# Performance work log

Hardware: AMD Instinct MI355X
Metric: run time of the kernel (lower is better)

Reference implementation:

```python
import jax, jax.numpy as jnp
import numpy as np

B_, N_, D_ = 8, 1024, 64
H_, DH_ = 4, 16
DI_, DS_, DTR_ = 128, 64, 4
MAXP = 512


def _ln(x, w, b, eps=1e-5):
    m = jnp.mean(x, -1, keepdims=True)
    v = jnp.mean((x - m) ** 2, -1, keepdims=True)
    return (x - m) * jax.lax.rsqrt(v + eps) * w + b


def _attn(x, drop_mask, Wq, Wkv, Wo, bo, rel_emb):
    b, n, d = x.shape
    scale = DH_ ** -0.5
    q = (x @ Wq).reshape(b, n, H_, DH_).transpose(0, 2, 1, 3)
    kv = x @ Wkv
    k = kv[..., :d].reshape(b, n, H_, DH_).transpose(0, 2, 1, 3)
    v = kv[..., d:].reshape(b, n, H_, DH_).transpose(0, 2, 1, 3)
    dots = jnp.einsum('bhid,bhjd->bhij', q, k) * scale
    seq = jnp.arange(n)
    dist = jnp.clip(seq[:, None] - seq[None, :], -MAXP, MAXP) + MAXP
    rpe = rel_emb[dist]  # (n, n, DH_)
    dots = dots + jnp.einsum('bhid,ijd->bhij', q, rpe) * scale
    # stochastic key drop: Bernoulli(0.3) positions get -1e12
    dots = dots + drop_mask.astype(dots.dtype) * (-1e12)
    attn = jax.nn.softmax(dots, axis=-1)
    out = jnp.einsum('bhij,bhjd->bhid', attn, v)
    out = out.transpose(0, 2, 1, 3).reshape(b, n, H_ * DH_)
    return out @ Wo + bo


def _mamba(x, W_in, conv_w, conv_b, W_xproj, W_dt, b_dt, A_log, Dm, W_out):
    b, n, _ = x.shape
    xz = x @ W_in                      # (b, n, 2*DI_)
    u, z = xz[..., :DI_], xz[..., DI_:]
    uc = u.transpose(0, 2, 1)          # (b, DI_, n)
    uc = jax.lax.conv_general_dilated(
        uc, conv_w[:, None, :], (1,), ((3, 0),),
        feature_group_count=DI_, dimension_numbers=('NCH', 'OIH', 'NCH'))
    uc = uc + conv_b[None, :, None]
    u = jax.nn.silu(uc).transpose(0, 2, 1)  # (b, n, DI_)
    xdb = u @ W_xproj                  # (b, n, DTR_+2*DS_)
    dt = jax.nn.softplus(xdb[..., :DTR_] @ W_dt + b_dt)  # (b, n, DI_)
    Bm = xdb[..., DTR_:DTR_ + DS_]
    Cm = xdb[..., DTR_ + DS_:]
    A = -jnp.exp(A_log)                # (DI_, DS_)

    def step(h, inp):
        dt_t, B_t, C_t, u_t = inp      # (b,DI_),(b,DS_),(b,DS_),(b,DI_)
        dA = jnp.exp(dt_t[..., None] * A)
        h = h * dA + (dt_t * u_t)[..., None] * B_t[:, None, :]
        y = jnp.einsum('bds,bs->bd', h, C_t)
        return h, y

    h0 = jnp.zeros((b, DI_, DS_), x.dtype)
    xs = (dt.transpose(1, 0, 2), Bm.transpose(1, 0, 2),
          Cm.transpose(1, 0, 2), u.transpose(1, 0, 2))
    _, ys = jax.lax.scan(step, h0, xs)
    y = ys.transpose(1, 0, 2) + u * Dm
    y = y * jax.nn.silu(z)
    return y @ W_out


def _rmsgn(x, gamma, eps=1e-5, groups=4):
    shp = x.shape
    dpg = shp[-1] // groups
    xg = x.reshape(shp[:-1] + (groups, dpg))
    rms = jnp.sqrt(jnp.sum(xg * xg, -1, keepdims=True)) * (dpg ** -0.5)
    return (xg / (rms + eps)).reshape(shp) * gamma


def _ff1(x, c1_w, c1_b, d1_w, d1_b):
    # SwiGLUConvDeconv1d(64, 256, kernel=4, shift=1); x: (b, s2, 64)
    s2 = x.shape[1]
    xc = x.transpose(0, 2, 1)
    xc = jnp.pad(xc, ((0, 0), (0, 0), (3, 3)))
    xc = jax.lax.conv_general_dilated(
        xc, c1_w, (1,), 'VALID', dimension_numbers=('NCH', 'OIH', 'NCH'))
    xc = xc + c1_b[None, :, None]
    gate = jax.nn.silu(xc[:, 256:, :])
    xc = xc[:, :256, :] * gate
    # ConvTranspose1d stride 1 == conv with flipped kernel, full padding
    w = jnp.flip(d1_w, -1).transpose(1, 0, 2)  # (64, 256, 4)
    xc = jax.lax.conv_general_dilated(
        xc, w, (1,), ((3, 3),), dimension_numbers=('NCH', 'OIH', 'NCH'))
    xc = xc + d1_b[None, :, None]
    out = xc.transpose(0, 2, 1)
    return out[:, 3:3 + s2, :]


def _forward(x, drop_mask, ln1_w, ln1_b, Wq, Wkv, Wo, bo, rel_emb,
             ln2_w, ln2_b, W_in, conv_w, conv_b, W_xproj, W_dt, b_dt,
             A_log, Dm, W_out, gamma, c1_w, c1_b, d1_w, d1_b, ln3_w, ln3_b):
    xt = _ln(x, ln1_w, ln1_b)
    xt = _attn(xt, drop_mask, Wq, Wkv, Wo, bo, rel_emb) + x
    x = x + xt  # dropout p=0 -> identity (faithful to original residual math)
    xt = _ln(x, ln2_w, ln2_b)
    m = _mamba(xt, W_in, conv_w, conv_b, W_xproj, W_dt, b_dt, A_log, Dm, W_out)
    m = jnp.where(m >= 0, m, 0.01 * m)  # leaky_relu
    m = _rmsgn(m, gamma)
    m = m + 0.5 * _ff1(m, c1_w, c1_b, d1_w, d1_b)
    x = x + m
    return _ln(x, ln3_w, ln3_b)


def setup_inputs() -> dict:
    ks = jax.random.split(jax.random.key(0), 16)
    g = lambda i, shp, s: jax.random.normal(ks[i], shp, dtype=jnp.float32) * s
    A_log = jnp.log(jnp.tile(jnp.arange(1, DS_ + 1, dtype=jnp.float32)[None, :], (DI_, 1)))
    return {
        'x': jax.random.normal(ks[0], (B_, N_, D_), dtype=jnp.float32),
        'drop_mask': jax.random.bernoulli(ks[1], 0.3, (B_, H_, N_, N_)),
        'ln1_w': jnp.ones((D_,), jnp.float32), 'ln1_b': jnp.zeros((D_,), jnp.float32),
        'Wq': g(2, (D_, D_), 0.1), 'Wkv': g(3, (D_, 2 * D_), 0.1),
        'Wo': g(4, (D_, D_), 0.1), 'bo': jnp.zeros((D_,), jnp.float32),
        'rel_emb': g(5, (2 * MAXP + 1, DH_), 0.02),
        'ln2_w': jnp.ones((D_,), jnp.float32), 'ln2_b': jnp.zeros((D_,), jnp.float32),
        'W_in': g(6, (D_, 2 * DI_), 0.1),
        'conv_w': g(7, (DI_, 4), 0.2), 'conv_b': jnp.zeros((DI_,), jnp.float32),
        'W_xproj': g(8, (DI_, DTR_ + 2 * DS_), 0.1),
        'W_dt': g(9, (DTR_, DI_), 0.1), 'b_dt': jnp.zeros((DI_,), jnp.float32),
        'A_log': A_log, 'Dm': jnp.ones((DI_,), jnp.float32),
        'W_out': g(10, (DI_, D_), 0.1),
        'gamma': jnp.ones((D_,), jnp.float32),
        'c1_w': g(11, (512, 64, 4), 0.1), 'c1_b': jnp.zeros((512,), jnp.float32),
        'd1_w': g(12, (256, 64, 4), 0.1), 'd1_b': jnp.zeros((64,), jnp.float32),
        'ln3_w': jnp.ones((D_,), jnp.float32), 'ln3_b': jnp.zeros((D_,), jnp.float32),
    }


def reference(x, drop_mask, ln1_w, ln1_b, Wq, Wkv, Wo, bo, rel_emb,
              ln2_w, ln2_b, W_in, conv_w, conv_b, W_xproj, W_dt, b_dt,
              A_log, Dm, W_out, gamma, c1_w, c1_b, d1_w, d1_b, ln3_w, ln3_b):
    return _forward(x, drop_mask, ln1_w, ln1_b, Wq, Wkv, Wo, bo, rel_emb,
                    ln2_w, ln2_b, W_in, conv_w, conv_b, W_xproj, W_dt, b_dt,
                    A_log, Dm, W_out, gamma, c1_w, c1_b, d1_w, d1_b, ln3_w, ln3_b)
```

## Files before the change

kernel.cpp:

```cpp
#include <hip/hip_runtime.h>
#include <hip/hip_fp16.h>
#include <math.h>


__device__ __forceinline__ float wsum64(float v){
#pragma unroll
  for(int m=32;m>0;m>>=1) v += __shfl_xor(v, m, 64);
  return v;
}
__device__ __forceinline__ float wmax64(float v){
#pragma unroll
  for(int m=32;m>0;m>>=1) v = fmaxf(v, __shfl_xor(v, m, 64));
  return v;
}
__device__ __forceinline__ float silu_f(float x){ return x / (1.f + __expf(-x)); }

__global__ __launch_bounds__(256) void k_ln1_qkv(
    const float* __restrict__ x, const float* __restrict__ w1, const float* __restrict__ b1,
    const float* __restrict__ Wq, const float* __restrict__ Wkv,
    const float* __restrict__ rel, const float* __restrict__ c1w,
    const int* __restrict__ dmask,
    float* __restrict__ qb, float2* __restrict__ kvT,
    float* __restrict__ relT, float* __restrict__ c1wT,
    unsigned long long* __restrict__ mask64){
  int tid = threadIdx.x;
  int bi = blockIdx.x >> 1;
  if (blockIdx.x & 1){
    size_t base = (size_t)bi * 16384;
    const int* dp = dmask + base;
    unsigned long long* mp = mask64 + (base >> 6);
#pragma unroll 4
    for(int r=0;r<64;++r){
      int m = dp[r*256 + tid];
      unsigned long long bal = __ballot(m != 0);
      if ((tid & 63) == 0) mp[r*4 + (tid >> 6)] = bal;
    }
    return;
  }
  int lane = tid & 63, warp = tid >> 6;
  int token = bi*4 + warp;
  __shared__ float xt[4][64];
  float xv = x[(size_t)token*64 + lane];
  float mean = wsum64(xv) * 0.015625f;
  float dlt = xv - mean;
  float var = wsum64(dlt*dlt) * 0.015625f;
  float xn = dlt * rsqrtf(var + 1e-5f) * w1[lane] + b1[lane];
  xt[warp][lane] = xn;
  __syncthreads();
  float aq=0.f, ak=0.f, av=0.f;
#pragma unroll 4
  for(int dd=0; dd<64; ++dd){
    float xd = xt[warp][dd];
    aq += xd * Wq[dd*64 + lane];
    ak += xd * Wkv[dd*128 + lane];
    av += xd * Wkv[dd*128 + 64 + lane];
  }
  int b = token >> 10, i = token & 1023;
  int h = lane >> 4, dh = lane & 15;
  size_t o  = (((size_t)(b*4 + h))*1024 + i)*16 + dh;
  size_t oT = (((size_t)(b*4 + h))*16 + dh)*1024 + i;
  qb[o]=aq;
  kvT[oT] = make_float2(ak, av);

  if (bi < 65){
    int idx = bi*256 + tid;
    if (idx < 16*1025){
      int c = idx / 1025;
      int d = idx - c*1025;
      relT[idx] = rel[d*16 + c];
    }
  } else if (bi < 577){
    int idx = (bi-65)*256 + tid;
    int row = idx >> 9;
    int ii  = idx & 511;
    c1wT[idx] = c1w[(size_t)ii*256 + row];
  }
}

__global__ __launch_bounds__(256) void k_kmax(
    const float2* __restrict__ kvT, float* __restrict__ Kmax){
  int tid = threadIdx.x;
  int bh = blockIdx.x;
  const float2* base = kvT + (size_t)bh*16*1024;
  float mx = 0.f;
#pragma unroll
  for(int r=0;r<4;++r){
    int j = tid + 256*r;
    float ss = 0.f;
#pragma unroll
    for(int c=0;c<16;++c){ float2 kv = base[c*1024 + j]; ss += kv.x*kv.x; }
    mx = fmaxf(mx, ss);
  }
  mx = wmax64(mx);
  __shared__ float red[4];
  int lane = tid&63, wv = tid>>6;
  if(lane==0) red[wv]=mx;
  __syncthreads();
  if(tid==0) Kmax[bh] = sqrtf(fmaxf(fmaxf(red[0],red[1]),fmaxf(red[2],red[3])));
}

__global__ __launch_bounds__(128, 2) void k_attn(
    const float* __restrict__ qb, const float2* __restrict__ kvT,
    const unsigned long long* __restrict__ mask64, const float* __restrict__ relT,
    const float* __restrict__ Kmax, float* __restrict__ attn_raw){
  int tid = threadIdx.x;
  int lane = tid & 63, wv = tid >> 6;
  int wg   = blockIdx.x;
  int xcd  = wg & 7;
  int slot = wg >> 3;
  int bh   = xcd*4 + (slot >> 7);
  int i0   = (slot & 127) * 8;
  int b = bh >> 2, h = bh & 3;
  int R0 = wv*4, R1 = R0+1, R2 = R0+2, R3 = R0+3;

  __shared__ __align__(16) __half Gc[8][1040];
  __shared__ float qs[8][16];
  __shared__ float G0s[8], G1024s[8];
  __shared__ float gmS[8];
  __shared__ float Ms[8];
  __shared__ float sums[8];

  {
    int r = tid >> 4, c = tid & 15;
    qs[r][c] = qb[((size_t)bh*1024 + i0 + r)*16 + c] * 0.25f;
  }
  __syncthreads();

#pragma unroll 1
  for(int bb=0; bb<9; ++bb){
    int d = tid + 128*bb;
    if (d <= 1024){
      float rl[16];
#pragma unroll
      for(int c=0;c<16;++c) rl[c] = relT[c*1025 + d];
#pragma unroll
      for(int r=0;r<8;++r){
        float g = 0.f;
#pragma unroll
        for(int c=0;c<16;++c) g += qs[r][c]*rl[c];
        if (d == 0)        G0s[r] = g;
        else if (d == 1024) G1024s[r] = g;
        else {
          int j = i0 + r + 512 - d;
          if (j >= 0 && j < 1024) Gc[r][j] = __float2half_rn(g);
        }
      }
    }
  }
  __syncthreads();
  {
    const unsigned long long* mrow = mask64 + ((size_t)bh*1024 + i0)*16;
#pragma unroll 1
    for(int r=0;r<8;++r){
      float g0 = G0s[r], g1 = G1024s[r];
      int lo = i0 + r - 512;
      int hi = i0 + r + 512;
#pragma unroll
      for(int p=0;p<8;++p){
        int j = tid + 128*p;
        unsigned long long w = mrow[r*16 + (j>>6)];
        float g;
        if (j >= hi) g = g0;
        else if (j <= lo) g = g1;
        else g = __half2float(Gc[r][j]);
        if ((w >> (j & 63)) & 1ULL) g = -60000.f;
        Gc[r][j] = __float2half_rn(g);
      }
    }
  }
  __syncthreads();
  {
    int r = tid >> 4, l4 = tid & 15;
    float gm = -3.0e38f;
#pragma unroll
    for(int k=0;k<64;++k) gm = fmaxf(gm, __half2float(Gc[r][l4 + 16*k]));
#pragma unroll
    for(int m=1;m<16;m<<=1) gm = fmaxf(gm, __shfl_xor(gm, m, 64));
    if (l4 == 0) gmS[r] = gm;
  }
  __syncthreads();
  if (tid < 8){
    float qn = 0.f;
#pragma unroll
    for(int c=0;c<16;++c) qn += qs[tid][c]*qs[tid][c];
    Ms[tid] = gmS[tid] + sqrtf(qn)*Kmax[bh];
  }
  __syncthreads();

  float q0[16], q1[16], q2[16], q3[16];
#pragma unroll
  for(int c=0;c<16;++c){ q0[c]=qs[R0][c]; q1[c]=qs[R1][c]; q2[c]=qs[R2][c]; q3[c]=qs[R3][c]; }
  float M0 = Ms[R0], M1 = Ms[R1], M2 = Ms[R2], M3 = Ms[R3];

  const float2* kvb = kvT + (size_t)bh*16*1024;

  float s0=0.f, s1=0.f, s2=0.f, s3=0.f;
  float a0[16], a1[16], a2[16], a3[16];
#pragma unroll
  for(int c=0;c<16;++c){ a0[c]=0.f; a1[c]=0.f; a2[c]=0.f; a3[c]=0.f; }

  float2 kvA[16], kvB[16];
  int j = lane;
#pragma unroll
  for(int c=0;c<16;++c) kvA[c] = kvb[c*1024 + j];

#define ATTN_STEP(KV, JJ) do {                                              \
    float sv0 = __half2float(Gc[R0][JJ]), sv1 = __half2float(Gc[R1][JJ]);   \
    float sv2 = __half2float(Gc[R2][JJ]), sv3 = __half2float(Gc[R3][JJ]);   \
    _Pragma("unroll")                                                       \
    for(int c=0;c<16;++c){                                                  \
      float kx = KV[c].x;                                                   \
      sv0 += q0[c]*kx; sv1 += q1[c]*kx; sv2 += q2[c]*kx; sv3 += q3[c]*kx;   \
    }                                                                       \
    float p0 = __expf(sv0 - M0), p1 = __expf(sv1 - M1);                     \
    float p2 = __expf(sv2 - M2), p3 = __expf(sv3 - M3);                     \
    s0 += p0; s1 += p1; s2 += p2; s3 += p3;                                 \
    _Pragma("unroll")                                                       \
    for(int c=0;c<16;++c){                                                  \
      float vy = KV[c].y;                                                   \
      a0[c] += p0*vy; a1[c] += p1*vy; a2[c] += p2*vy; a3[c] += p3*vy;       \
    }                                                                       \
  } while(0)

#pragma unroll 1
  for(int t=0;t<16;t+=2){
    int jb = (j + 64) & 1023;
#pragma unroll
    for(int c=0;c<16;++c) kvB[c] = kvb[c*1024 + jb];
    ATTN_STEP(kvA, j);
    int ja = (jb + 64) & 1023;
#pragma unroll
    for(int c=0;c<16;++c) kvA[c] = kvb[c*1024 + ja];
    ATTN_STEP(kvB, jb);
    j = ja;
  }
#undef ATTN_STEP

  s0 = wsum64(s0); s1 = wsum64(s1); s2 = wsum64(s2); s3 = wsum64(s3);
#pragma unroll
  for(int c=0;c<16;++c){
    float x0 = a0[c]; x0 += __shfl_xor(x0,32,64); x0 += __shfl_xor(x0,16,64); a0[c] = x0;
    float x1 = a1[c]; x1 += __shfl_xor(x1,32,64); x1 += __shfl_xor(x1,16,64); a1[c] = x1;
    float x2 = a2[c]; x2 += __shfl_xor(x2,32,64); x2 += __shfl_xor(x2,16,64); a2[c] = x2;
    float x3 = a3[c]; x3 += __shfl_xor(x3,32,64); x3 += __shfl_xor(x3,16,64); a3[c] = x3;
  }
  __syncthreads();
  float* red = (float*)&Gc[0][0];
  if (lane < 16){
#pragma unroll
    for(int c=0;c<16;++c){
      red[R0*272 + lane*17 + c] = a0[c];
      red[R1*272 + lane*17 + c] = a1[c];
      red[R2*272 + lane*17 + c] = a2[c];
      red[R3*272 + lane*17 + c] = a3[c];
    }
  }
  if (lane == 0){ sums[R0]=s0; sums[R1]=s1; sums[R2]=s2; sums[R3]=s3; }
  __syncthreads();
  {
    int row = tid >> 4, c = tid & 15;
    float tot = 0.f;
#pragma unroll
    for(int g=0; g<16; ++g) tot += red[row*272 + g*17 + c];
    attn_raw[((size_t)b*1024 + i0 + row)*64 + h*16 + c] = tot / sums[row];
  }
}

__global__ __launch_bounds__(256) void k_post_attn(
    const float* __restrict__ x, const float* __restrict__ attn_raw,
    const float* __restrict__ Wo, const float* __restrict__ bo,
    const float* __restrict__ ln2w, const float* __restrict__ ln2b,
    const float* __restrict__ W_in,
    float* __restrict__ x2, float* __restrict__ u0, float* __restrict__ zsarr){
  int tid = threadIdx.x;
  int lane = tid & 63, wv = tid >> 6;
  int tok0 = blockIdx.x * 16;
  __shared__ float arS[16][64];
  __shared__ float lnS[16][64];
  for(int l = tid; l < 1024; l += 256)
    arS[l >> 6][l & 63] = attn_raw[(size_t)tok0*64 + l];
  __syncthreads();
#pragma unroll 1
  for(int tt = 0; tt < 4; ++tt){
    int tl = wv*4 + tt;
    int token = tok0 + tl;
    float acc = bo[lane];
#pragma unroll 4
    for(int dd = 0; dd < 64; ++dd) acc += arS[tl][dd] * Wo[dd*64 + lane];
    float t = 2.f*x[(size_t)token*64 + lane] + acc;
    x2[(size_t)token*64 + lane] = t;
    float mean = wsum64(t)*0.015625f;
    float dlt = t - mean;
    float var = wsum64(dlt*dlt)*0.015625f;
    lnS[tl][lane] = dlt*rsqrtf(var+1e-5f)*ln2w[lane] + ln2b[lane];
  }
  __syncthreads();
  int oc = tid;
  float w[64];
#pragma unroll
  for(int dd = 0; dd < 64; ++dd) w[dd] = W_in[dd*256 + oc];
  const float4* lnS4 = (const float4*)&lnS[0][0];
#pragma unroll 1
  for(int tl = 0; tl < 16; ++tl){
    float acc = 0.f;
#pragma unroll
    for(int d4 = 0; d4 < 16; ++d4){
      float4 l4 = lnS4[tl*16 + d4];
      acc += l4.x*w[4*d4] + l4.y*w[4*d4+1] + l4.z*w[4*d4+2] + l4.w*w[4*d4+3];
    }
    int token = tok0 + tl;
    if (oc < 128) u0[(size_t)token*128 + oc] = acc;
    else          zsarr[(size_t)token*128 + (oc-128)] = silu_f(acc);
  }
}

__global__ __launch_bounds__(256) void k_conv_proj(
    const float* __restrict__ u0, const float* __restrict__ conv_w, const float* __restrict__ conv_b,
    const float* __restrict__ W_xproj, const float* __restrict__ W_dt, const float* __restrict__ b_dt,
    float* __restrict__ uarr, float* __restrict__ Bmp, float* __restrict__ Cmp, float* __restrict__ dtarr){
  int sub = threadIdx.x >> 7, c = threadIdx.x & 127;
  int token = blockIdx.x*2 + sub;
  int b = token >> 10, i = token & 1023;
  __shared__ float us[2][128];
  __shared__ float dtin[2][4];
  float acc = conv_b[c];
#pragma unroll
  for(int k2=0;k2<4;++k2){
    int t2 = i - 3 + k2;
    if (t2 >= 0) acc += u0[((size_t)b*1024 + t2)*128 + c]*conv_w[c*4+k2];
  }
  float uv = silu_f(acc);
  uarr[(size_t)token*128 + c] = uv;
  us[sub][c] = uv;
  __syncthreads();
  float accA = 0.f, accB = 0.f;
  int cB = 128 + (c & 3);
#pragma unroll 4
  for(int dd=0; dd<128; ++dd){
    float xd = us[sub][dd];
    accA += xd * W_xproj[dd*132 + c];
    accB += xd * W_xproj[dd*132 + cB];
  }
  if (c < 4){ dtin[sub][c] = accA; Cmp[(size_t)token*64 + 60 + c] = accB; }
  else if (c < 68) Bmp[(size_t)token*64 + (c-4)] = accA;
  else             Cmp[(size_t)token*64 + (c-68)] = accA;
  __syncthreads();
  float dv = b_dt[c];
#pragma unroll
  for(int r2=0;r2<4;++r2) dv += dtin[sub][r2]*W_dt[r2*128 + c];
  dv = fmaxf(dv, 0.f) + log1pf(expf(-fabsf(dv)));
  dtarr[(size_t)token*128 + c] = dv;
}

__global__ __launch_bounds__(256) void k_scan_a(
    const float* __restrict__ dtarr, const float* __restrict__ uarr,
    const float* __restrict__ Bmp, const float* __restrict__ A_log,
    float* __restrict__ Parr, float* __restrict__ Rarr){
  int lane = threadIdx.x & 63, warp = threadIdx.x >> 6;
  int wgid = blockIdx.x;
  int b = wgid & 7;
  int slot = wgid >> 3;
  int d = slot & 127;
  int c = (slot >> 7)*4 + warp;
  size_t pw = (size_t)b*1024 + d*8 + c;
  float A = -expf(A_log[d*64 + lane]);
  int tb = c*128;
  const float* dtp = dtarr + ((size_t)b*1024 + tb)*128 + d;
  const float* up  = uarr  + ((size_t)b*1024 + tb)*128 + d;
  const float* Bp  = Bmp   + ((size_t)b*1024 + tb)*64 + lane;
  float R = 0.f, sdt = 0.f;
  for(int t0=0; t0<128; t0+=8){
    float dtc[8], uc[8], Bc[8];
#pragma unroll
    for(int r=0;r<8;++r){
      dtc[r]=dtp[(size_t)(t0+r)*128]; uc[r]=up[(size_t)(t0+r)*128]; Bc[r]=Bp[(size_t)(t0+r)*64];
    }
#pragma unroll
    for(int r=0;r<8;++r){
      float dt = dtc[r];
      R = R*__expf(dt*A) + dt*uc[r]*Bc[r];
      sdt += dt;
    }
  }
  Parr[pw*64 + lane] = __expf(sdt*A);
  Rarr[pw*64 + lane] = R;
}

__global__ __launch_bounds__(256) void k_scan_c(
    const float* __restrict__ dtarr, const float* __restrict__ uarr,
    const float* __restrict__ Bmp, const float* __restrict__ Cmp,
    const float* __restrict__ zsarr, const float* __restrict__ A_log,
    const float* __restrict__ Dm, const float* __restrict__ Parr,
    const float* __restrict__ Rarr, float* __restrict__ ymp){
  int lane = threadIdx.x & 63, warp = threadIdx.x >> 6;
  int wgid = blockIdx.x;
  int b = wgid & 7;
  int slot = wgid >> 3;
  int d = slot & 127;
  int c = (slot >> 7)*4 + warp;
  size_t pbase = (size_t)b*1024 + d*8;
  float A = -expf(A_log[d*64 + lane]);
  float Dv = Dm[d];
  float h = 0.f;
#pragma unroll 1
  for(int cp=0; cp<c; ++cp){
    float P = Parr[(pbase+cp)*64 + lane];
    float R = Rarr[(pbase+cp)*64 + lane];
    h = h*P + R;
  }
  int tb = c*128;
  const float* dtp = dtarr + ((size_t)b*1024 + tb)*128 + d;
  const float* up  = uarr  + ((size_t)b*1024 + tb)*128 + d;
  const float* zp  = zsarr + ((size_t)b*1024 + tb)*128 + d;
  const float* Bp  = Bmp   + ((size_t)b*1024 + tb)*64 + lane;
  const float* Cp  = Cmp   + ((size_t)b*1024 + tb)*64 + lane;
  float* yp        = ymp   + ((size_t)b*1024 + tb)*128 + d;
  for(int t0=0; t0<128; t0+=8){
    float dtc[8], uc[8], Bc[8], Cc[8], zc[8];
#pragma unroll
    for(int r=0;r<8;++r){
      dtc[r]=dtp[(size_t)(t0+r)*128]; uc[r]=up[(size_t)(t0+r)*128];
      Bc[r]=Bp[(size_t)(t0+r)*64];    Cc[r]=Cp[(size_t)(t0+r)*64];
      zc[r]=zp[(size_t)(t0+r)*128];
    }
    float hc[8];
#pragma unroll
    for(int r=0;r<8;++r){
      float dt = dtc[r];
      h = h*__expf(dt*A) + dt*uc[r]*Bc[r];
      hc[r] = h*Cc[r];
    }
    float y[8];
#pragma unroll
    for(int r=0;r<8;++r) y[r] = wsum64(hc[r]);
    if (lane==0){
#pragma unroll
      for(int r=0;r<8;++r) yp[(size_t)(t0+r)*128] = (y[r] + uc[r]*Dv)*zc[r];
    }
  }
}

__global__ __launch_bounds__(256) void k_wout(
    const float* __restrict__ ymp, const float* __restrict__ W_out,
    const float* __restrict__ gamma, float* __restrict__ marr){
  int lane = threadIdx.x & 63, warp = threadIdx.x >> 6;
  int token = blockIdx.x*4 + warp;
  __shared__ float ys[4][128];
  ys[warp][lane]      = ymp[(size_t)token*128 + lane];
  ys[warp][lane+64]   = ymp[(size_t)token*128 + 64 + lane];
  __syncthreads();
  float acc = 0.f;
#pragma unroll 4
  for(int dd=0; dd<128; ++dd) acc += ys[warp][dd]*W_out[dd*64 + lane];
  acc = acc >= 0.f ? acc : 0.01f*acc;
  float ss = acc*acc;
#pragma unroll
  for(int m=1;m<16;m<<=1) ss += __shfl_xor(ss, m, 64);
  float rms = sqrtf(ss)*0.25f;
  marr[(size_t)token*64 + lane] = acc/(rms + 1e-5f)*gamma[lane];
}

__global__ __launch_bounds__(256) void k_h2(
    const float* __restrict__ marr, const float* __restrict__ c1wT,
    const float* __restrict__ c1b, float* __restrict__ h2){
  int b = blockIdx.y;
  int t0 = blockIdx.x * 16;
  int tid = threadIdx.x;
  __shared__ float ms[19][64];
  for(int l = tid; l < 19*64; l += 256){
    int row = l >> 6, cc = l & 63;
    int t = t0 - 3 + row;
    ms[row][cc] = (t >= 0 && t < 1024) ? marr[((size_t)b*1024 + t)*64 + cc] : 0.f;
  }
  __syncthreads();
  int i = tid;
  float acc1[16], acc2[16];
#pragma unroll
  for(int tl=0;tl<16;++tl){ acc1[tl]=0.f; acc2[tl]=0.f; }
  for(int cc=0; cc<64; ++cc){
    float mv[19];
#pragma unroll
    for(int r2=0;r2<19;++r2) mv[r2] = ms[r2][cc];
    const float* wr = c1wT + (size_t)cc*4*512;
    float wa0 = wr[      i], wa1 = wr[ 512+i], wa2 = wr[1024+i], wa3 = wr[1536+i];
    float wg0 = wr[  256+i], wg1 = wr[ 768+i], wg2 = wr[1280+i], wg3 = wr[1792+i];
#pragma unroll
    for(int tl=0; tl<16; ++tl){
      acc1[tl] += wa0*mv[tl+0] + wa1*mv[tl+1] + wa2*mv[tl+2] + wa3*mv[tl+3];
      acc2[tl] += wg0*mv[tl+0] + wg1*mv[tl+1] + wg2*mv[tl+2] + wg3*mv[tl+3];
    }
  }
  float bb1 = c1b[i], bb2 = c1b[i+256];
#pragma unroll
  for(int tl=0; tl<16; ++tl){
    int t = t0 + tl;
    if (t < 1027){
      float o1 = acc1[tl] + bb1;
      float o2 = acc2[tl] + bb2;
      h2[((size_t)b*1027 + t)*256 + i] = o1 * silu_f(o2);
    }
  }
}

__global__ __launch_bounds__(256) void k_ff_final(
    const float* __restrict__ h2, const float* __restrict__ d1w, const float* __restrict__ d1b,
    const float* __restrict__ x2, const float* __restrict__ marr,
    const float* __restrict__ ln3w, const float* __restrict__ ln3b,
    float* __restrict__ out){
  int b = blockIdx.y;
  int s0 = blockIdx.x * 16;
  int tid = threadIdx.x;
  int o = tid & 63, sg = tid >> 6;
  __shared__ float hs[19][256];
  for(int l = tid; l < 19*256; l += 256){
    int row = l >> 8, cc = l & 255;
    hs[row][cc] = h2[((size_t)b*1027 + s0 + row)*256 + cc];
  }
  __syncthreads();
  int sl = sg*4;
  float acc0=0.f, acc1=0.f, acc2=0.f, acc3=0.f;
  const float4* wb = (const float4*)d1w + o;
#pragma unroll 2
  for(int i2=0; i2<256; ++i2){
    float4 wv = wb[(size_t)i2*64];
    float h0=hs[sl+0][i2], h1=hs[sl+1][i2], h2v=hs[sl+2][i2], h3=hs[sl+3][i2];
    float h4=hs[sl+4][i2], h5=hs[sl+5][i2], h6=hs[sl+6][i2];
    acc0 += h0*wv.w + h1*wv.z + h2v*wv.y + h3*wv.x;
    acc1 += h1*wv.w + h2v*wv.z + h3*wv.y + h4*wv.x;
    acc2 += h2v*wv.w + h3*wv.z + h4*wv.y + h5*wv.x;
    acc3 += h3*wv.w + h4*wv.z + h5*wv.y + h6*wv.x;
  }
  float accs[4] = {acc0, acc1, acc2, acc3};
  float bo_ = d1b[o];
#pragma unroll
  for(int r=0;r<4;++r){
    int s = s0 + sl + r;
    size_t idx = ((size_t)b*1024 + s)*64 + o;
    float tot = x2[idx] + marr[idx] + 0.5f*(accs[r] + bo_);
    float mean = wsum64(tot)*0.015625f;
    float dlt = tot - mean;
    float var = wsum64(dlt*dlt)*0.015625f;
    out[idx] = dlt*rsqrtf(var+1e-5f)*ln3w[o] + ln3b[o];
  }
}

extern "C" void kernel_launch(void* const* d_in, const int* in_sizes, int n_in,
                              void* d_out, int out_size, void* d_ws, size_t ws_size,
                              hipStream_t stream){
  const float* x       = (const float*)d_in[0];
  const int*   dmask   = (const int*)  d_in[1];
  const float* ln1w    = (const float*)d_in[2];
  const float* ln1b    = (const float*)d_in[3];
  const float* Wq      = (const float*)d_in[4];
  const float* Wkv     = (const float*)d_in[5];
  const float* Wo      = (const float*)d_in[6];
  const float* bo      = (const float*)d_in[7];
  const float* rel     = (const float*)d_in[8];
  const float* ln2w    = (const float*)d_in[9];
  const float* ln2b    = (const float*)d_in[10];
  const float* W_in    = (const float*)d_in[11];
  const float* conv_w  = (const float*)d_in[12];
  const float* conv_b  = (const float*)d_in[13];
  const float* W_xproj = (const float*)d_in[14];
  const float* W_dt    = (const float*)d_in[15];
  const float* b_dt    = (const float*)d_in[16];
  const float* A_log   = (const float*)d_in[17];
  const float* Dm      = (const float*)d_in[18];
  const float* W_out   = (const float*)d_in[19];
  const float* gamma   = (const float*)d_in[20];
  const float* c1w     = (const float*)d_in[21];
  const float* c1b     = (const float*)d_in[22];
  const float* d1w     = (const float*)d_in[23];
  const float* d1b     = (const float*)d_in[24];
  const float* ln3w    = (const float*)d_in[25];
  const float* ln3b    = (const float*)d_in[26];
  float* outp = (float*)d_out;

  float* ws = (float*)d_ws;
  float* qb       = ws;
  float* kvT      = qb      + 524288;
  float* attn_raw = kvT     + 1048576;
  float* x2       = attn_raw+ 524288;
  float* u0       = x2      + 524288;
  float* zsarr    = u0      + 1048576;
  float* uarr     = zsarr   + 1048576;
  float* dtarr    = uarr    + 1048576;
  float* Bmp      = dtarr   + 1048576;
  float* Cmp      = Bmp     + 524288;
  float* ymp      = Cmp     + 524288;
  float* marr     = ymp     + 1048576;
  float* h2       = marr    + 524288;
  float* relT     = h2      + 2103296;
  float* c1wT     = relT    + 16400;
  float* Parr     = c1wT    + 131072;
  float* Rarr     = Parr    + 524288;
  float* Kmaxa    = Rarr    + 524288;

  unsigned long long* mask64 = (unsigned long long*)h2;

  k_ln1_qkv  <<<4096, 256, 0, stream>>>(x, ln1w, ln1b, Wq, Wkv, rel, c1w, dmask,
                                        qb, (float2*)kvT, relT, c1wT, mask64);
  k_kmax     <<<32, 256, 0, stream>>>((const float2*)kvT, Kmaxa);
  k_attn     <<<4096, 128, 0, stream>>>(qb, (const float2*)kvT, mask64, relT, Kmaxa, attn_raw);
  k_post_attn<<<512, 256, 0, stream>>>(x, attn_raw, Wo, bo, ln2w, ln2b, W_in, x2, u0, zsarr);
  k_conv_proj<<<4096, 256, 0, stream>>>(u0, conv_w, conv_b, W_xproj, W_dt, b_dt, uarr, Bmp, Cmp, dtarr);
  k_scan_a   <<<2048, 256, 0, stream>>>(dtarr, uarr, Bmp, A_log, Parr, Rarr);
  k_scan_c   <<<2048, 256, 0, stream>>>(dtarr, uarr, Bmp, Cmp, zsarr, A_log, Dm, Parr, Rarr, ymp);
  k_wout     <<<2048, 256, 0, stream>>>(ymp, W_out, gamma, marr);
  k_h2       <<<dim3(65,8), 256, 0, stream>>>(marr, c1wT, c1b, h2);
  k_ff_final <<<dim3(64,8), 256, 0, stream>>>(h2, d1w, d1b, x2, marr, ln3w, ln3b, outp);
}
```

Measured before the change: 763.4 us.

## Double the attention tile to 16 query rows and stage K/V through LDS

The attention kernel now handles 16 query rows per 256-thread workgroup instead of 8 rows per 128 threads, halving the grid. K/V chunks are loaded cooperatively into double-buffered shared memory, so four waves reuse each chunk instead of each wave loading it from global memory itself. The relative-position bias pass is rewritten so each wave computes four rows with query values held in wave-uniform registers via readfirstlane. This cuts redundant global K/V traffic, at the cost of a barrier per chunk, more LDS use per workgroup, and possibly lower occupancy.

After: 714.9 us. 6.4% less time.

```diff
diff --git a/kernel.cpp b/kernel.cpp
--- a/kernel.cpp
+++ b/kernel.cpp
@@ -14,6 +14,9 @@
   return v;
 }
 __device__ __forceinline__ float silu_f(float x){ return x / (1.f + __expf(-x)); }
+__device__ __forceinline__ float rfl_f(float x){
+  return __int_as_float(__builtin_amdgcn_readfirstlane(__float_as_int(x)));
+}
 
 __global__ __launch_bounds__(256) void k_ln1_qkv(
     const float* __restrict__ x, const float* __restrict__ w1, const float* __restrict__ b1,
@@ -99,26 +102,29 @@
   if(tid==0) Kmax[bh] = sqrtf(fmaxf(fmaxf(red[0],red[1]),fmaxf(red[2],red[3])));
 }
 
-__global__ __launch_bounds__(128, 2) void k_attn(
+__global__ __launch_bounds__(256, 2) void k_attn(
     const float* __restrict__ qb, const float2* __restrict__ kvT,
     const unsigned long long* __restrict__ mask64, const float* __restrict__ relT,
     const float* __restrict__ Kmax, float* __restrict__ attn_raw){
   int tid = threadIdx.x;
-  int lane = tid & 63, wv = tid >> 6;
+  int lane = tid & 63;
+  int wvu  = __builtin_amdgcn_readfirstlane(tid >> 6);
   int wg   = blockIdx.x;
   int xcd  = wg & 7;
   int slot = wg >> 3;
-  int bh   = xcd*4 + (slot >> 7);
-  int i0   = (slot & 127) * 8;
+  int bh   = xcd*4 + (slot >> 6);
+  int i0   = (slot & 63) * 16;
   int b = bh >> 2, h = bh & 3;
-  int R0 = wv*4, R1 = R0+1, R2 = R0+2, R3 = R0+3;
-
-  __shared__ __align__(16) __half Gc[8][1040];
-  __shared__ float qs[8][16];
-  __shared__ float G0s[8], G1024s[8];
-  __shared__ float gmS[8];
-  __shared__ float Ms[8];
-  __shared__ float sums[8];
+  int R0 = wvu*4, R1 = R0+1, R2 = R0+2, R3 = R0+3;
+
+  __shared__ __align__(16) __half Gc[16][1040];
+  __shared__ float kvX[2][16][64];
+  __shared__ float kvY[2][16][64];
+  __shared__ float qs[16][16];
+  __shared__ float G0s[16], G1024s[16];
+  __shared__ float gmS[16];
+  __shared__ float Ms[16];
+  __shared__ float sums[16];
 
   {
     int r = tid >> 4, c = tid & 15;
@@ -126,24 +132,48 @@
   }
   __syncthreads();
 
+  float q0[16], q1[16], q2[16], q3[16];
+#pragma unroll
+  for(int c=0;c<16;++c){
+    q0[c]=rfl_f(qs[R0][c]); q1[c]=rfl_f(qs[R1][c]);
+    q2[c]=rfl_f(qs[R2][c]); q3[c]=rfl_f(qs[R3][c]);
+  }
+
+  const float2* kvb = kvT + (size_t)bh*16*1024;
+  float2 st[4];
+#define LOADREGS(CH) do{ int _j0=(CH)*64;                                   \
+    _Pragma("unroll")                                                       \
+    for(int k=0;k<4;++k){ int idx=tid+256*k; int c=idx>>6, jl=idx&63;       \
+      st[k]=kvb[c*1024 + _j0 + jl]; } }while(0)
+#define WRITEB(NB) do{                                                      \
+    _Pragma("unroll")                                                       \
+    for(int k=0;k<4;++k){ int idx=tid+256*k; int c=idx>>6, jl=idx&63;       \
+      kvX[NB][c][jl]=st[k].x; kvY[NB][c][jl]=st[k].y; } }while(0)
+
+  LOADREGS(0);
+
 #pragma unroll 1
-  for(int bb=0; bb<9; ++bb){
-    int d = tid + 128*bb;
+  for(int bb=0; bb<17; ++bb){
+    int d = lane + 64*bb;
     if (d <= 1024){
       float rl[16];
 #pragma unroll
       for(int c=0;c<16;++c) rl[c] = relT[c*1025 + d];
-#pragma unroll
-      for(int r=0;r<8;++r){
-        float g = 0.f;
-#pragma unroll
-        for(int c=0;c<16;++c) g += qs[r][c]*rl[c];
-        if (d == 0)        G0s[r] = g;
-        else if (d == 1024) G1024s[r] = g;
-        else {
-          int j = i0 + r + 512 - d;
-          if (j >= 0 && j < 1024) Gc[r][j] = __float2half_rn(g);
-        }
+      float g0=0.f, g1=0.f, g2=0.f, g3=0.f;
+#pragma unroll
+      for(int c=0;c<16;++c){
+        float rc = rl[c];
+        g0 += q0[c]*rc; g1 += q1[c]*rc; g2 += q2[c]*rc; g3 += q3[c]*rc;
+      }
+      if (d == 0){ G0s[R0]=g0; G0s[R1]=g1; G0s[R2]=g2; G0s[R3]=g3; }
+      else if (d == 1024){ G1024s[R0]=g0; G1024s[R1]=g1; G1024s[R2]=g2; G1024s[R3]=g3; }
+      else {
+        int base = i0 + 512 - d;
+        int j0r = base + R0;
+        if (j0r+0 >= 0 && j0r+0 < 1024) Gc[R0][j0r+0] = __float2half_rn(g0);
+        if (j0r+1 >= 0 && j0r+1 < 1024) Gc[R1][j0r+1] = __float2half_rn(g1);
+        if (j0r+2 >= 0 && j0r+2 < 1024) Gc[R2][j0r+2] = __float2half_rn(g2);
+        if (j0r+3 >= 0 && j0r+3 < 1024) Gc[R3][j0r+3] = __float2half_rn(g3);
       }
     }
   }
@@ -151,13 +181,13 @@
   {
     const unsigned long long* mrow = mask64 + ((size_t)bh*1024 + i0)*16;
 #pragma unroll 1
-    for(int r=0;r<8;++r){
+    for(int r=0;r<16;++r){
       float g0 = G0s[r], g1 = G1024s[r];
       int lo = i0 + r - 512;
       int hi = i0 + r + 512;
 #pragma unroll
-      for(int p=0;p<8;++p){
-        int j = tid + 128*p;
+      for(int p=0;p<4;++p){
+        int j = tid + 256*p;
         unsigned long long w = mrow[r*16 + (j>>6)];
         float g;
         if (j >= hi) g = g0;
@@ -179,7 +209,7 @@
     if (l4 == 0) gmS[r] = gm;
   }
   __syncthreads();
-  if (tid < 8){
+  if (tid < 16){
     float qn = 0.f;
 #pragma unroll
     for(int c=0;c<16;++c) qn += qs[tid][c]*qs[tid][c];
@@ -187,54 +217,46 @@
   }
   __syncthreads();
 
-  float q0[16], q1[16], q2[16], q3[16];
-#pragma unroll
-  for(int c=0;c<16;++c){ q0[c]=qs[R0][c]; q1[c]=qs[R1][c]; q2[c]=qs[R2][c]; q3[c]=qs[R3][c]; }
-  float M0 = Ms[R0], M1 = Ms[R1], M2 = Ms[R2], M3 = Ms[R3];
-
-  const float2* kvb = kvT + (size_t)bh*16*1024;
+  float M0 = rfl_f(Ms[R0]), M1 = rfl_f(Ms[R1]);
+  float M2 = rfl_f(Ms[R2]), M3 = rfl_f(Ms[R3]);
 
   float s0=0.f, s1=0.f, s2=0.f, s3=0.f;
   float a0[16], a1[16], a2[16], a3[16];
 #pragma unroll
   for(int c=0;c<16;++c){ a0[c]=0.f; a1[c]=0.f; a2[c]=0.f; a3[c]=0.f; }
 
-  float2 kvA[16], kvB[16];
-  int j = lane;
-#pragma unroll
-  for(int c=0;c<16;++c) kvA[c] = kvb[c*1024 + j];
-
-#define ATTN_STEP(KV, JJ) do {                                              \
-    float sv0 = __half2float(Gc[R0][JJ]), sv1 = __half2float(Gc[R1][JJ]);   \
-    float sv2 = __half2float(Gc[R2][JJ]), sv3 = __half2float(Gc[R3][JJ]);   \
-    _Pragma("unroll")                                                       \
-    for(int c=0;c<16;++c){                                                  \
-      float kx = KV[c].x;                                                   \
-      sv0 += q0[c]*kx; sv1 += q1[c]*kx; sv2 += q2[c]*kx; sv3 += q3[c]*kx;   \
-    }                                                                       \
-    float p0 = __expf(sv0 - M0), p1 = __expf(sv1 - M1);                     \
-    float p2 = __expf(sv2 - M2), p3 = __expf(sv3 - M3);                     \
-    s0 += p0; s1 += p1; s2 += p2; s3 += p3;                                 \
-    _Pragma("unroll")                                                       \
-    for(int c=0;c<16;++c){                                                  \
-      float vy = KV[c].y;                                                   \
-      a0[c] += p0*vy; a1[c] += p1*vy; a2[c] += p2*vy; a3[c] += p3*vy;       \
-    }                                                                       \
-  } while(0)
+  WRITEB(0);
+  LOADREGS(1);
+  __syncthreads();
+  int cur = 0;
 
 #pragma unroll 1
-  for(int t=0;t<16;t+=2){
-    int jb = (j + 64) & 1023;
-#pragma unroll
-    for(int c=0;c<16;++c) kvB[c] = kvb[c*1024 + jb];
-    ATTN_STEP(kvA, j);
-    int ja = (jb + 64) & 1023;
-#pragma unroll
-    for(int c=0;c<16;++c) kvA[c] = kvb[c*1024 + ja];
-    ATTN_STEP(kvB, jb);
-    j = ja;
-  }
-#undef ATTN_STEP
+  for(int ch=0; ch<16; ++ch){
+    int j = ch*64 + lane;
+    float sv0 = __half2float(Gc[R0][j]), sv1 = __half2float(Gc[R1][j]);
+    float sv2 = __half2float(Gc[R2][j]), sv3 = __half2float(Gc[R3][j]);
+#pragma unroll
+    for(int c=0;c<16;++c){
+      float kxc = kvX[cur][c][lane];
+      sv0 += q0[c]*kxc; sv1 += q1[c]*kxc; sv2 += q2[c]*kxc; sv3 += q3[c]*kxc;
+    }
+    float p0 = __expf(sv0 - M0), p1 = __expf(sv1 - M1);
+    float p2 = __expf(sv2 - M2), p3 = __expf(sv3 - M3);
+    s0 += p0; s1 += p1; s2 += p2; s3 += p3;
+#pragma unroll
+    for(int c=0;c<16;++c){
+      float vyc = kvY[cur][c][lane];
+      a0[c] += p0*vyc; a1[c] += p1*vyc; a2[c] += p2*vyc; a3[c] += p3*vyc;
+    }
+    if (ch < 15){
+      WRITEB(cur^1);
+      if (ch < 14) LOADREGS(ch+2);
+    }
+    __syncthreads();
+    cur ^= 1;
+  }
+#undef LOADREGS
+#undef WRITEB
 
   s0 = wsum64(s0); s1 = wsum64(s1); s2 = wsum64(s2); s3 = wsum64(s3);
 #pragma unroll
@@ -601,7 +623,7 @@
   k_ln1_qkv  <<<4096, 256, 0, stream>>>(x, ln1w, ln1b, Wq, Wkv, rel, c1w, dmask,
                                         qb, (float2*)kvT, relT, c1wT, mask64);
   k_kmax     <<<32, 256, 0, stream>>>((const float2*)kvT, Kmaxa);
-  k_attn     <<<4096, 128, 0, stream>>>(qb, (const float2*)kvT, mask64, relT, Kmaxa, attn_raw);
+  k_attn     <<<2048, 256, 0, stream>>>(qb, (const float2*)kvT, mask64, relT, Kmaxa, attn_raw);
   k_post_attn<<<512, 256, 0, stream>>>(x, attn_raw, Wo, bo, ln2w, ln2b, W_in, x2, u0, zsarr);
   k_conv_proj<<<4096, 256, 0, stream>>>(u0, conv_w, conv_b, W_xproj, W_dt, b_dt, uarr, Bmp, Cmp, dtarr);
   k_scan_a   <<<2048, 256, 0, stream>>>(dtarr, uarr, Bmp, A_log, Parr, Rarr);
```
